# Performance work log

Hardware: AMD Instinct MI355X
Metric: run time of the kernel (lower is better)

The kernel has to match this reference:

```python
import jax, jax.numpy as jnp
import numpy as np

ALPHA = 1.0
GAMMA = 0.8
TAU = 0.1
NUM_SAMPLES = 10
TOP_K = 100
NUM_USER_GROUPS = 8
NUM_ITEM_GROUPS = 16
BATCH = 1024
NUM_ITEMS = 10000


def setup_inputs() -> dict:
    key = jax.random.key(0)
    k1, k2, k3, k4 = jax.random.split(key, 4)
    pred_scores = jax.random.normal(k1, (BATCH, NUM_ITEMS), dtype=jnp.float32)
    true_scores = jax.random.uniform(k2, (BATCH, NUM_ITEMS), dtype=jnp.float32)
    user_groups = jax.random.randint(k3, (BATCH,), 0, NUM_USER_GROUPS)
    item_groups = jax.random.randint(k4, (NUM_ITEMS,), 0, NUM_ITEM_GROUPS)
    return {
        "pred_scores": pred_scores,
        "true_scores": true_scores,
        "user_groups": user_groups,
        "item_groups": item_groups,
    }


def _calculate_exposure(scores):
    # scores: [B, k]. Soft-rank via Gumbel perturbations + pairwise sigmoid.
    B, k = scores.shape
    noise = jax.random.gumbel(jax.random.key(1), (NUM_SAMPLES, B, k), dtype=scores.dtype)
    noisy = scores[None, :, :] + noise                       # [S, B, k]
    diffs = noisy[..., :, None] - noisy[..., None, :]        # [S, B, k, k]
    # ranks = 1 + sum_j sigmoid((s_i - s_j)/tau) - sigmoid(0)
    ranks = 1.0 + jax.nn.sigmoid(diffs / TAU).sum(axis=-1) - 0.5  # [S, B, k]
    exposure = jnp.power(GAMMA, ranks - 1.0)                 # [S, B, k]
    return exposure.mean(axis=0)                             # [B, k]


def reference(pred_scores, true_scores, user_groups, item_groups):
    B = pred_scores.shape[0]
    # top-k selection (values == gathered pred scores)
    pred_topk, topk_idx = jax.lax.top_k(pred_scores, TOP_K)   # [B, k]
    item_groups_topk = item_groups[topk_idx]                  # [B, k]

    system_exposure = _calculate_exposure(pred_topk)          # [B, k]
    target_exposure = jnp.full_like(system_exposure, true_scores.mean())
    delta_E = system_exposure - target_exposure               # [B, k]

    ii_f_loss = jnp.mean(delta_E * delta_E)

    # group-pair scatter_mean
    pair_ids = user_groups[:, None] * NUM_ITEM_GROUPS + item_groups_topk  # [B, k]
    flat = delta_E.reshape(-1)
    pid = pair_ids.reshape(-1)
    num_pairs = NUM_USER_GROUPS * NUM_ITEM_GROUPS
    sums = jax.ops.segment_sum(flat, pid, num_segments=num_pairs)
    cnts = jax.ops.segment_sum(jnp.ones_like(flat), pid, num_segments=num_pairs)
    avg = jnp.where(cnts > 0, sums / jnp.maximum(cnts, 1.0), 0.0)
    gg_f_loss = jnp.mean(avg * avg)

    total_loss = ii_f_loss + ALPHA * gg_f_loss
    return (total_loss, ii_f_loss, gg_f_loss)
```

## Files before the change

### kernel.cpp

```cpp
#include <hip/hip_runtime.h>


typedef unsigned int u32;
typedef unsigned long long u64;

__device__ __forceinline__ u32 rotl32(u32 x, int r) { return (x << r) | (x >> (32 - r)); }

__device__ __forceinline__ void tf2x32(u32 k0, u32 k1, u32 x0, u32 x1, u32& o0, u32& o1) {
  u32 ks2 = 0x1BD11BDAu ^ k0 ^ k1;
#define TFR(r) { x0 += x1; x1 = rotl32(x1, r); x1 ^= x0; }
  x0 += k0; x1 += k1;
  TFR(13) TFR(15) TFR(26) TFR(6)
  x0 += k1; x1 += ks2 + 1u;
  TFR(17) TFR(29) TFR(16) TFR(24)
  x0 += ks2; x1 += k0 + 2u;
  TFR(13) TFR(15) TFR(26) TFR(6)
  x0 += k0; x1 += k1 + 3u;
  TFR(17) TFR(29) TFR(16) TFR(24)
  x0 += k1; x1 += ks2 + 4u;
  TFR(13) TFR(15) TFR(26) TFR(6)
  x0 += ks2; x1 += k0 + 5u;
#undef TFR
  o0 = x0; o1 = x1;
}

__device__ __forceinline__ float gumbel_noise(u32 i) {
  u32 o0, o1;
  tf2x32(0u, 1u, 0u, i, o0, o1);
  u32 bits = o0 ^ o1;
  float f = __uint_as_float((bits >> 9) | 0x3f800000u) - 1.0f;
  const float TINY = 1.17549435e-38f;
  float u = fmaxf(TINY, f + TINY);
  return -logf(-logf(u));
}

__device__ __forceinline__ u32 fkey(float v) {
  u32 u = __float_as_uint(v);
  return u ^ ((u & 0x80000000u) ? 0xFFFFFFFFu : 0x80000000u);
}

__device__ __forceinline__ void select_bin(const u32* __restrict__ hist, int shift,
                                           u32* sh_T, u32* sh_A, u32* sh_done,
                                           int lane) {
  u32 prevA = *sh_A;
  u32 target = 100u - prevA;
  u32 c0 = hist[lane * 4 + 0], c1 = hist[lane * 4 + 1];
  u32 c2 = hist[lane * 4 + 2], c3 = hist[lane * 4 + 3];
  u32 s = c0 + c1 + c2 + c3;
  u32 suf = s;
#pragma unroll
  for (int off = 1; off < 64; off <<= 1) {
    u32 o = __shfl_down(suf, off);
    suf += (lane + off < 64) ? o : 0u;
  }
  u32 sufx = suf - s;
  if (sufx < target && suf >= target) {
    u32 cc[4] = {c0, c1, c2, c3};
    u32 acc = sufx, bin = 0, cnt = 0;
#pragma unroll
    for (int k = 3; k >= 0; --k) {
      if (acc + cc[k] >= target) { bin = (u32)(lane * 4 + k); cnt = cc[k]; break; }
      acc += cc[k];
    }
    u32 newA = prevA + acc;
    *sh_T = *sh_T | (bin << shift);
    *sh_A = newA;
    *sh_done = (newA + cnt <= 128u || shift == 0) ? 1u : 0u;
  }
}

__global__ __launch_bounds__(512, 8) void fused_kernel(
    const float* __restrict__ pred,
    const float* __restrict__ ts,
    const int*   __restrict__ ugrp,
    const int*   __restrict__ igrp,
    double* __restrict__ t_sum,
    double* __restrict__ sum_e, double* __restrict__ sum_e2,
    double* __restrict__ pair_sum, int* __restrict__ pair_cnt) {
  const int N = 10000, N4 = 2500, K = 100;
  const int b = blockIdx.x;
  const int t = threadIdx.x;

  __shared__ u32 hist4[4][256];
  __shared__ u64 cand[2048];
  __shared__ u64 sbuf[128];
  __shared__ u64 sorted[128];
  __shared__ u32 rankv[128];
  __shared__ float topv[100];
  __shared__ int   pidv[100];
  __shared__ __align__(16) float noisy[1000];
  __shared__ float expo[100];
  __shared__ float pairS[128];
  __shared__ int   pairC[128];
  __shared__ float wred[8];
  __shared__ u32 sh_cnt, sh_nc, sh_T, sh_A, sh_done, sh_ovf;
  __shared__ float sh_bS, sh_bS2;

  if (t < 256) { hist4[0][t] = 0u; hist4[1][t] = 0u; hist4[2][t] = 0u; hist4[3][t] = 0u; }
  if (t < 128) { pairS[t] = 0.f; pairC[t] = 0; rankv[t] = 0u; }
  if (t < 100) expo[t] = 0.f;
  if (t == 0) { sh_cnt = 0u; sh_nc = 0u; sh_T = 0u; sh_A = 0u; sh_done = 0u; sh_ovf = 0u;
                sh_bS = 0.f; sh_bS2 = 0.f; }
  __syncthreads();

  const float4* __restrict__ row4 = (const float4*)(pred + (size_t)b * N);
  const float4* __restrict__ tsr4 = (const float4*)(ts + (size_t)b * N);

  float tsum = 0.f;
  u32* myh = hist4[(t >> 7) & 3];
#pragma unroll
  for (int k = 0; k < 5; ++k) {
    int i4 = t + (k << 9);
    if (k == 4 && i4 >= N4) break;
    float4 pp = row4[i4];
    float4 qq = tsr4[i4];
    tsum += (qq.x + qq.y) + (qq.z + qq.w);
    atomicAdd(&myh[fkey(pp.x) >> 24], 1u);
    atomicAdd(&myh[fkey(pp.y) >> 24], 1u);
    atomicAdd(&myh[fkey(pp.z) >> 24], 1u);
    atomicAdd(&myh[fkey(pp.w) >> 24], 1u);
  }
#pragma unroll
  for (int off = 32; off; off >>= 1) tsum += __shfl_down(tsum, off);
  if ((t & 63) == 0) wred[t >> 6] = tsum;
  __syncthreads();
  if (t == 0) {
    float s8 = 0.f;
#pragma unroll
    for (int w = 0; w < 8; ++w) s8 += wred[w];
    atomicAdd(t_sum, (double)s8);
  }
  if (t < 256) hist4[0][t] += hist4[1][t] + hist4[2][t] + hist4[3][t];
  __syncthreads();

  if (t < 64) select_bin(&hist4[0][0], 24, &sh_T, &sh_A, &sh_done, t);
  __syncthreads();

  bool r1done = (sh_done != 0u);
  bool use_cand = false;
  u32 nc = 0;

  if (!r1done) {
    u32 b0 = sh_T >> 24;
    for (int i4 = t; i4 < N4; i4 += 512) {
      float4 pp = row4[i4];
#pragma unroll
      for (int c = 0; c < 4; ++c) {
        float v = (c == 0) ? pp.x : (c == 1) ? pp.y : (c == 2) ? pp.z : pp.w;
        u32 key = fkey(v);
        if ((key >> 24) >= b0) {
          u32 pos = atomicAdd(&sh_cnt, 1u);
          int idx = i4 * 4 + c;
          if (pos < 2048u) cand[pos] = ((u64)key << 32) | (u32)(~(u32)idx);
          else sh_ovf = 1u;
        }
      }
    }
    __syncthreads();
    nc = sh_cnt < 2048u ? sh_cnt : 2048u;
    use_cand = (sh_ovf == 0u);

    for (int shift = 16; ; shift -= 8) {
      if (t < 256) hist4[0][t] = 0u;
      __syncthreads();
      u32 pref = sh_T >> (shift + 8);
      if (use_cand) {
        for (int i = t; i < (int)nc; i += 512) {
          u32 key = (u32)(cand[i] >> 32);
          if ((key >> (shift + 8)) == pref) atomicAdd(&hist4[0][(key >> shift) & 255u], 1u);
        }
      } else {
        for (int i4 = t; i4 < N4; i4 += 512) {
          float4 pp = row4[i4];
#pragma unroll
          for (int c = 0; c < 4; ++c) {
            float v = (c == 0) ? pp.x : (c == 1) ? pp.y : (c == 2) ? pp.z : pp.w;
            u32 key = fkey(v);
            if ((key >> (shift + 8)) == pref) atomicAdd(&hist4[0][(key >> shift) & 255u], 1u);
          }
        }
      }
      __syncthreads();
      if (t < 64) select_bin(&hist4[0][0], shift, &sh_T, &sh_A, &sh_done, t);
      __syncthreads();
      if (sh_done) break;
    }
  }

  {
    u32 T = sh_T;
    if (use_cand) {
      for (int i = t; i < (int)nc; i += 512) {
        u64 p = cand[i];
        if ((u32)(p >> 32) >= T) {
          u32 pos = atomicAdd(&sh_nc, 1u);
          if (pos < 128u) sbuf[pos] = p;
        }
      }
    } else {
      for (int i4 = t; i4 < N4; i4 += 512) {
        float4 pp = row4[i4];
#pragma unroll
        for (int c = 0; c < 4; ++c) {
          float v = (c == 0) ? pp.x : (c == 1) ? pp.y : (c == 2) ? pp.z : pp.w;
          u32 key = fkey(v);
          if (key >= T) {
            u32 pos = atomicAdd(&sh_nc, 1u);
            int idx = i4 * 4 + c;
            if (pos < 128u) sbuf[pos] = ((u64)key << 32) | (u32)(~(u32)idx);
          }
        }
      }
    }
    __syncthreads();
    u32 nreal = sh_nc < 128u ? sh_nc : 128u;
    if (t < 128 && (u32)t >= nreal) sbuf[t] = 0ull;
    __syncthreads();
  }

  {
    int e = t >> 2, seg = t & 3;
    u64 mykey = sbuf[e];
    u32 cnt = 0;
    int j0 = seg * 32;
#pragma unroll 8
    for (int j = j0; j < j0 + 32; ++j) cnt += (sbuf[j] > mykey) ? 1u : 0u;
    if (cnt) atomicAdd(&rankv[e], cnt);
    __syncthreads();
    if (t < 128) sorted[rankv[t]] = sbuf[t];
    __syncthreads();
  }

  int ug = ugrp[b];
  if (t < K) {
    u64 pk = sorted[t];
    u32 key = (u32)(pk >> 32);
    u32 idx = ~(u32)pk;
    u32 u = (key & 0x80000000u) ? (key ^ 0x80000000u) : ~key;
    topv[t] = __uint_as_float(u);
    pidv[t] = ug * 16 + igrp[idx];
  }
  __syncthreads();

  for (int si = t; si < 1000; si += 512) {
    int s = si / 100, i = si - s * 100;
    noisy[si] = topv[i] + gumbel_noise(((u32)s * 1024u + (u32)b) * 100u + (u32)i);
  }
  __syncthreads();

  const float C2 = 14.426950408889634f;
  const float LG = -0.32192809488736235f;
  for (int si = t; si < 1000; si += 512) {
    int s = si / 100, i = si - s * 100;
    float nvC = noisy[si] * C2;
    const float4* nr4 = (const float4*)(noisy + s * 100);
    float S = 0.f;
#pragma unroll 5
    for (int jc = 0; jc < 25; ++jc) {
      float4 nj = nr4[jc];
      S += __builtin_amdgcn_rcpf(1.0f + exp2f(__builtin_fmaf(nj.x, C2, -nvC)));
      S += __builtin_amdgcn_rcpf(1.0f + exp2f(__builtin_fmaf(nj.y, C2, -nvC)));
      S += __builtin_amdgcn_rcpf(1.0f + exp2f(__builtin_fmaf(nj.z, C2, -nvC)));
      S += __builtin_amdgcn_rcpf(1.0f + exp2f(__builtin_fmaf(nj.w, C2, -nvC)));
    }
    float ex = exp2f((S - 0.5f) * LG);
    atomicAdd(&expo[i], ex);
  }
  __syncthreads();

  if (t < K) {
    float e = expo[t] * 0.1f;
    atomicAdd(&pairS[pidv[t]], e);
    atomicAdd(&pairC[pidv[t]], 1);
    atomicAdd(&sh_bS, e);
    atomicAdd(&sh_bS2, e * e);
  }
  __syncthreads();
  if (t < 128 && pairC[t] > 0) {
    atomicAdd(&pair_sum[t], (double)pairS[t]);
    atomicAdd(&pair_cnt[t], pairC[t]);
  }
  if (t == 0) {
    atomicAdd(sum_e, (double)sh_bS);
    atomicAdd(sum_e2, (double)sh_bS2);
  }
}

__global__ __launch_bounds__(128) void finalize_kernel(
    const double* __restrict__ t_sum, const double* __restrict__ sum_e,
    const double* __restrict__ sum_e2, const double* __restrict__ pair_sum,
    const int* __restrict__ pair_cnt, float* __restrict__ out) {
  int t = threadIdx.x;
  __shared__ double red[128];
  double tmean = *t_sum / 10240000.0;
  double g = 0.0;
  int c = pair_cnt[t];
  if (c > 0) {
    double avg = (pair_sum[t] - (double)c * tmean) / (double)c;
    g = avg * avg;
  }
  red[t] = g;
  __syncthreads();
#pragma unroll
  for (int off = 64; off; off >>= 1) {
    if (t < off) red[t] += red[t + off];
    __syncthreads();
  }
  if (t == 0) {
    double gg = red[0] / 128.0;
    double me = *sum_e / 102400.0;
    double me2 = *sum_e2 / 102400.0;
    double ii = me2 - 2.0 * tmean * me + tmean * tmean;
    out[0] = (float)(ii + gg);
    out[1] = (float)ii;
    out[2] = (float)gg;
  }
}

extern "C" void kernel_launch(void* const* d_in, const int* in_sizes, int n_in,
                              void* d_out, int out_size, void* d_ws, size_t ws_size,
                              hipStream_t stream) {
  (void)in_sizes; (void)n_in; (void)out_size; (void)ws_size;
  const float* pred = (const float*)d_in[0];
  const float* ts   = (const float*)d_in[1];
  const int*   ugrp = (const int*)d_in[2];
  const int*   igrp = (const int*)d_in[3];
  float* out = (float*)d_out;

  double* t_sum    = (double*)d_ws;
  double* sum_e    = t_sum + 1;
  double* sum_e2   = t_sum + 2;
  double* pair_sum = t_sum + 3;
  int*    pair_cnt = (int*)(t_sum + 3 + 128);

  hipMemsetAsync(d_ws, 0, (3 + 128) * sizeof(double) + 128 * sizeof(int), stream);

  fused_kernel<<<1024, 512, 0, stream>>>(pred, ts, ugrp, igrp,
                                         t_sum, sum_e, sum_e2, pair_sum, pair_cnt);
  finalize_kernel<<<1, 128, 0, stream>>>(t_sum, sum_e, sum_e2, pair_sum, pair_cnt, out);
}
```

Baseline: 167.8 us.

## Prefilter top-k candidates with fixed threshold and split selection from exposure kernel

The first pass over each row now collects candidates whose key is at or above a fixed threshold (values ≥ 2.0) instead of building a full 256-bin histogram with per-element shared atomics. The radix select then runs only over that small candidate list, with a full-row fallback when the count is below 100 or the buffer overflows. The fused kernel is also split into a selection kernel and an exposure kernel that pass the sorted key/index pairs through workspace, which reduces shared memory per kernel. In exchange there is an extra launch and a global round trip, and the fast path depends on how the input values are distributed.

```diff
diff --git a/kernel.cpp b/kernel.cpp
--- a/kernel.cpp
+++ b/kernel.cpp
@@ -69,45 +69,34 @@
   }
 }
 
-__global__ __launch_bounds__(512, 8) void fused_kernel(
+#define KSTAT 0xC0000000u
+
+__global__ __launch_bounds__(512, 8) void selection_kernel(
     const float* __restrict__ pred,
     const float* __restrict__ ts,
-    const int*   __restrict__ ugrp,
-    const int*   __restrict__ igrp,
     double* __restrict__ t_sum,
-    double* __restrict__ sum_e, double* __restrict__ sum_e2,
-    double* __restrict__ pair_sum, int* __restrict__ pair_cnt) {
-  const int N = 10000, N4 = 2500, K = 100;
+    u64* __restrict__ keyidx_ws) {
+  const int N4 = 2500, K = 100;
   const int b = blockIdx.x;
   const int t = threadIdx.x;
 
-  __shared__ u32 hist4[4][256];
   __shared__ u64 cand[2048];
+  __shared__ u32 hist[256];
   __shared__ u64 sbuf[128];
   __shared__ u64 sorted[128];
   __shared__ u32 rankv[128];
-  __shared__ float topv[100];
-  __shared__ int   pidv[100];
-  __shared__ __align__(16) float noisy[1000];
-  __shared__ float expo[100];
-  __shared__ float pairS[128];
-  __shared__ int   pairC[128];
   __shared__ float wred[8];
-  __shared__ u32 sh_cnt, sh_nc, sh_T, sh_A, sh_done, sh_ovf;
-  __shared__ float sh_bS, sh_bS2;
-
-  if (t < 256) { hist4[0][t] = 0u; hist4[1][t] = 0u; hist4[2][t] = 0u; hist4[3][t] = 0u; }
-  if (t < 128) { pairS[t] = 0.f; pairC[t] = 0; rankv[t] = 0u; }
-  if (t < 100) expo[t] = 0.f;
-  if (t == 0) { sh_cnt = 0u; sh_nc = 0u; sh_T = 0u; sh_A = 0u; sh_done = 0u; sh_ovf = 0u;
-                sh_bS = 0.f; sh_bS2 = 0.f; }
-  __syncthreads();
-
-  const float4* __restrict__ row4 = (const float4*)(pred + (size_t)b * N);
-  const float4* __restrict__ tsr4 = (const float4*)(ts + (size_t)b * N);
+  __shared__ u32 sh_cnt, sh_nc, sh_T, sh_A, sh_done;
+
+  if (t < 256) hist[t] = 0u;
+  if (t < 128) rankv[t] = 0u;
+  if (t == 0) { sh_cnt = 0u; sh_nc = 0u; sh_T = 0u; sh_A = 0u; sh_done = 0u; }
+  __syncthreads();
+
+  const float4* __restrict__ row4 = (const float4*)(pred + (size_t)b * 10000);
+  const float4* __restrict__ tsr4 = (const float4*)(ts + (size_t)b * 10000);
 
   float tsum = 0.f;
-  u32* myh = hist4[(t >> 7) & 3];
 #pragma unroll
   for (int k = 0; k < 5; ++k) {
     int i4 = t + (k << 9);
@@ -115,10 +104,16 @@
     float4 pp = row4[i4];
     float4 qq = tsr4[i4];
     tsum += (qq.x + qq.y) + (qq.z + qq.w);
-    atomicAdd(&myh[fkey(pp.x) >> 24], 1u);
-    atomicAdd(&myh[fkey(pp.y) >> 24], 1u);
-    atomicAdd(&myh[fkey(pp.z) >> 24], 1u);
-    atomicAdd(&myh[fkey(pp.w) >> 24], 1u);
+#pragma unroll
+    for (int c = 0; c < 4; ++c) {
+      float v = (c == 0) ? pp.x : (c == 1) ? pp.y : (c == 2) ? pp.z : pp.w;
+      u32 key = fkey(v);
+      if (key >= KSTAT) {
+        u32 pos = atomicAdd(&sh_cnt, 1u);
+        int idx = i4 * 4 + c;
+        if (pos < 2048u) cand[pos] = ((u64)key << 32) | (u32)(~(u32)idx);
+      }
+    }
   }
 #pragma unroll
   for (int off = 32; off; off >>= 1) tsum += __shfl_down(tsum, off);
@@ -130,93 +125,73 @@
     for (int w = 0; w < 8; ++w) s8 += wred[w];
     atomicAdd(t_sum, (double)s8);
   }
-  if (t < 256) hist4[0][t] += hist4[1][t] + hist4[2][t] + hist4[3][t];
-  __syncthreads();
-
-  if (t < 64) select_bin(&hist4[0][0], 24, &sh_T, &sh_A, &sh_done, t);
-  __syncthreads();
-
-  bool r1done = (sh_done != 0u);
-  bool use_cand = false;
-  u32 nc = 0;
-
-  if (!r1done) {
-    u32 b0 = sh_T >> 24;
+
+  u32 cnt_all = sh_cnt;
+  bool fast = (cnt_all >= 100u && cnt_all <= 2048u);
+  u32 nc = cnt_all < 2048u ? cnt_all : 2048u;
+
+  if (fast) {
+    for (int shift = 24; ; shift -= 8) {
+      if (t < 256) hist[t] = 0u;
+      __syncthreads();
+      u32 pref = sh_T >> (shift + 8);
+      for (int i = t; i < (int)nc; i += 512) {
+        u32 key = (u32)(cand[i] >> 32);
+        if (shift == 24 || (key >> (shift + 8)) == pref)
+          atomicAdd(&hist[(key >> shift) & 255u], 1u);
+      }
+      __syncthreads();
+      if (t < 64) select_bin(hist, shift, &sh_T, &sh_A, &sh_done, t);
+      __syncthreads();
+      if (sh_done) break;
+    }
+    u32 T = sh_T;
+    for (int i = t; i < (int)nc; i += 512) {
+      u64 p = cand[i];
+      if ((u32)(p >> 32) >= T) {
+        u32 pos = atomicAdd(&sh_nc, 1u);
+        if (pos < 128u) sbuf[pos] = p;
+      }
+    }
+  } else {
+    for (int shift = 24; ; shift -= 8) {
+      if (t < 256) hist[t] = 0u;
+      __syncthreads();
+      u32 pref = sh_T >> (shift + 8);
+      for (int i4 = t; i4 < N4; i4 += 512) {
+        float4 pp = row4[i4];
+#pragma unroll
+        for (int c = 0; c < 4; ++c) {
+          float v = (c == 0) ? pp.x : (c == 1) ? pp.y : (c == 2) ? pp.z : pp.w;
+          u32 key = fkey(v);
+          if (shift == 24 || (key >> (shift + 8)) == pref)
+            atomicAdd(&hist[(key >> shift) & 255u], 1u);
+        }
+      }
+      __syncthreads();
+      if (t < 64) select_bin(hist, shift, &sh_T, &sh_A, &sh_done, t);
+      __syncthreads();
+      if (sh_done) break;
+    }
+    u32 T = sh_T;
     for (int i4 = t; i4 < N4; i4 += 512) {
       float4 pp = row4[i4];
 #pragma unroll
       for (int c = 0; c < 4; ++c) {
         float v = (c == 0) ? pp.x : (c == 1) ? pp.y : (c == 2) ? pp.z : pp.w;
         u32 key = fkey(v);
-        if ((key >> 24) >= b0) {
-          u32 pos = atomicAdd(&sh_cnt, 1u);
+        if (key >= T) {
+          u32 pos = atomicAdd(&sh_nc, 1u);
           int idx = i4 * 4 + c;
-          if (pos < 2048u) cand[pos] = ((u64)key << 32) | (u32)(~(u32)idx);
-          else sh_ovf = 1u;
+          if (pos < 128u) sbuf[pos] = ((u64)key << 32) | (u32)(~(u32)idx);
         }
       }
     }
-    __syncthreads();
-    nc = sh_cnt < 2048u ? sh_cnt : 2048u;
-    use_cand = (sh_ovf == 0u);
-
-    for (int shift = 16; ; shift -= 8) {
-      if (t < 256) hist4[0][t] = 0u;
-      __syncthreads();
-      u32 pref = sh_T >> (shift + 8);
-      if (use_cand) {
-        for (int i = t; i < (int)nc; i += 512) {
-          u32 key = (u32)(cand[i] >> 32);
-          if ((key >> (shift + 8)) == pref) atomicAdd(&hist4[0][(key >> shift) & 255u], 1u);
-        }
-      } else {
-        for (int i4 = t; i4 < N4; i4 += 512) {
-          float4 pp = row4[i4];
-#pragma unroll
-          for (int c = 0; c < 4; ++c) {
-            float v = (c == 0) ? pp.x : (c == 1) ? pp.y : (c == 2) ? pp.z : pp.w;
-            u32 key = fkey(v);
-            if ((key >> (shift + 8)) == pref) atomicAdd(&hist4[0][(key >> shift) & 255u], 1u);
-          }
-        }
-      }
-      __syncthreads();
-      if (t < 64) select_bin(&hist4[0][0], shift, &sh_T, &sh_A, &sh_done, t);
-      __syncthreads();
-      if (sh_done) break;
-    }
-  }
-
-  {
-    u32 T = sh_T;
-    if (use_cand) {
-      for (int i = t; i < (int)nc; i += 512) {
-        u64 p = cand[i];
-        if ((u32)(p >> 32) >= T) {
-          u32 pos = atomicAdd(&sh_nc, 1u);
-          if (pos < 128u) sbuf[pos] = p;
-        }
-      }
-    } else {
-      for (int i4 = t; i4 < N4; i4 += 512) {
-        float4 pp = row4[i4];
-#pragma unroll
-        for (int c = 0; c < 4; ++c) {
-          float v = (c == 0) ? pp.x : (c == 1) ? pp.y : (c == 2) ? pp.z : pp.w;
-          u32 key = fkey(v);
-          if (key >= T) {
-            u32 pos = atomicAdd(&sh_nc, 1u);
-            int idx = i4 * 4 + c;
-            if (pos < 128u) sbuf[pos] = ((u64)key << 32) | (u32)(~(u32)idx);
-          }
-        }
-      }
-    }
-    __syncthreads();
-    u32 nreal = sh_nc < 128u ? sh_nc : 128u;
-    if (t < 128 && (u32)t >= nreal) sbuf[t] = 0ull;
-    __syncthreads();
-  }
+  }
+  __syncthreads();
+  u32 nreal = sh_nc < 128u ? sh_nc : 128u;
+  if (t < 128 && (u32)t >= nreal) sbuf[t] = 0ull;
+  __syncthreads();
 
   {
     int e = t >> 2, seg = t & 3;
@@ -231,9 +206,32 @@
     __syncthreads();
   }
 
+  if (t < K) keyidx_ws[(size_t)b * K + t] = sorted[t];
+}
+
+__global__ __launch_bounds__(512, 8) void expo_kernel(
+    const u64* __restrict__ keyidx_ws,
+    const int* __restrict__ ugrp, const int* __restrict__ igrp,
+    double* __restrict__ sum_e, double* __restrict__ sum_e2,
+    double* __restrict__ pair_sum, int* __restrict__ pair_cnt) {
+  const int K = 100;
+  const int b = blockIdx.x;
+  const int t = threadIdx.x;
+
+  __shared__ float topv[100];
+  __shared__ int   pidv[100];
+  __shared__ __align__(16) float noisy[1000];
+  __shared__ float expo[100];
+  __shared__ float pairS[128];
+  __shared__ int   pairC[128];
+  __shared__ float sh_bS, sh_bS2;
+
+  if (t < 128) { pairS[t] = 0.f; pairC[t] = 0; }
+  if (t < 100) expo[t] = 0.f;
+  if (t == 0) { sh_bS = 0.f; sh_bS2 = 0.f; }
   int ug = ugrp[b];
   if (t < K) {
-    u64 pk = sorted[t];
+    u64 pk = keyidx_ws[(size_t)b * K + t];
     u32 key = (u32)(pk >> 32);
     u32 idx = ~(u32)pk;
     u32 u = (key & 0x80000000u) ? (key ^ 0x80000000u) : ~key;
@@ -332,10 +330,12 @@
   double* sum_e2   = t_sum + 2;
   double* pair_sum = t_sum + 3;
   int*    pair_cnt = (int*)(t_sum + 3 + 128);
+  u64*    keyidx   = (u64*)((char*)d_ws + (3 + 128) * sizeof(double) + 128 * sizeof(int));
 
   hipMemsetAsync(d_ws, 0, (3 + 128) * sizeof(double) + 128 * sizeof(int), stream);
 
-  fused_kernel<<<1024, 512, 0, stream>>>(pred, ts, ugrp, igrp,
-                                         t_sum, sum_e, sum_e2, pair_sum, pair_cnt);
+  selection_kernel<<<1024, 512, 0, stream>>>(pred, ts, t_sum, keyidx);
+  expo_kernel<<<1024, 512, 0, stream>>>(keyidx, ugrp, igrp,
+                                        sum_e, sum_e2, pair_sum, pair_cnt);
   finalize_kernel<<<1, 128, 0, stream>>>(t_sum, sum_e, sum_e2, pair_sum, pair_cnt, out);
 }
```

After: 168.3 us. About the same (+0.3%).
